# Kernel tuning notes

Measured on AMD Instinct MI355X. Metric: run time of the kernel, lower is better.

The kernel has to match this reference:

```python
import jax, jax.numpy as jnp
import numpy as np

H = 16  # num_attention_heads


def setup_inputs() -> dict:
    key = jax.random.key(0)
    ks = jax.random.split(key, 4)
    B, S, D = 2, 2048, 1024
    hidden_states = jax.random.normal(ks[0], (B, S, D), dtype=jnp.float32)
    attention_mask = jnp.zeros((B, 1, 1, S), dtype=jnp.float32)
    scale = 1.0 / np.sqrt(D)
    Wq = jax.random.normal(ks[1], (D, D), dtype=jnp.float32) * scale
    Wk = jax.random.normal(ks[2], (D, D), dtype=jnp.float32) * scale
    Wv = jax.random.normal(ks[3], (D, D), dtype=jnp.float32) * scale
    bq = jnp.zeros((D,), dtype=jnp.float32)
    bk = jnp.zeros((D,), dtype=jnp.float32)
    bv = jnp.zeros((D,), dtype=jnp.float32)
    return {"hidden_states": hidden_states, "attention_mask": attention_mask,
            "Wq": Wq, "bq": bq, "Wk": Wk, "bk": bk, "Wv": Wv, "bv": bv}


def reference(hidden_states, attention_mask, Wq, bq, Wk, bk, Wv, bv):
    B, S, D = hidden_states.shape
    Dh = D // H

    def proj(W, b):
        # torch Linear: x @ W.T + b ; reshape to [B, H, S, Dh]
        y = jnp.einsum('bsd,ed->bse', hidden_states, W) + b
        return y.reshape(B, S, H, Dh).transpose(0, 2, 1, 3)

    q = proj(Wq, bq)
    k = proj(Wk, bk)
    v = proj(Wv, bv)

    scores = jnp.einsum('bhqd,bhkd->bhqk', q, k) / jnp.sqrt(jnp.float32(Dh))
    scores = scores + attention_mask  # additive mask broadcast [B,1,1,S]
    probs = jax.nn.softmax(scores, axis=-1)  # [B,H,Sq,Sk]
    out_attention_scores = probs.sum(axis=-2).sum(axis=-2)  # [B, Sk]
    # dropout prob = 0 (eval) -> identity
    context = jnp.einsum('bhqk,bhkd->bhqd', probs, v)
    context = context.transpose(0, 2, 1, 3).reshape(B, S, D)
    return context, out_attention_scores
```

## Files before the change

### kernel.cpp

```cpp
#include <hip/hip_runtime.h>
#include <hip/hip_bf16.h>
#include <stdint.h>

typedef unsigned short u16;
typedef __attribute__((ext_vector_type(8))) unsigned short u16x8;
typedef __attribute__((ext_vector_type(4))) unsigned short u16x4;
typedef __attribute__((ext_vector_type(8))) __bf16 bf16x8;
typedef __attribute__((ext_vector_type(4))) float f32x4;
typedef __attribute__((ext_vector_type(16))) float f32x16;

#define LOG2E 1.44269504088896340736f

#if defined(__has_builtin)
#if __has_builtin(__builtin_amdgcn_exp2f)
#define EXP2(x) __builtin_amdgcn_exp2f(x)
#endif
#endif
#ifndef EXP2
#define EXP2(x) exp2f(x)
#endif

__device__ __forceinline__ f32x4 mfma16(u16x8 a, u16x8 b, f32x4 c) {
  return __builtin_amdgcn_mfma_f32_16x16x32_bf16(
      __builtin_bit_cast(bf16x8, a), __builtin_bit_cast(bf16x8, b), c, 0, 0, 0);
}

__device__ __forceinline__ f32x16 mfma32(u16x8 a, u16x8 b, f32x16 c) {
  return __builtin_amdgcn_mfma_f32_32x32x16_bf16(
      __builtin_bit_cast(bf16x8, a), __builtin_bit_cast(bf16x8, b), c, 0, 0, 0);
}

__device__ __forceinline__ u16 f2bf(float f) {
  unsigned u = __builtin_bit_cast(unsigned, f);
  return (u16)((u + 0x7fffu + ((u >> 16) & 1u)) >> 16);
}

__device__ __forceinline__ unsigned cvtpk(float a, float b) {
  unsigned r;
  asm volatile("v_cvt_pk_bf16_f32 %0, %1, %2" : "=v"(r) : "v"(a), "v"(b));
  return r;
}

__device__ __forceinline__ void pswap(unsigned& a, unsigned& b) {
  asm volatile("v_permlane32_swap_b32 %0, %1" : "+v"(a), "+v"(b));
}

__device__ __forceinline__ void gload_lds16(const void* g, void* l) {
  __builtin_amdgcn_global_load_lds(
      (__attribute__((address_space(1))) void*)const_cast<void*>(g),
      (__attribute__((address_space(3))) void*)l, 16, 0, 0);
}

template<int N> __device__ __forceinline__ void vmwait() {
  __builtin_amdgcn_sched_barrier(0);
  asm volatile("s_waitcnt vmcnt(%0)" :: "n"(N) : "memory");
  __builtin_amdgcn_sched_barrier(0);
}

#define SWZ(row, colbyte) ((((row) * 128) + (colbyte)) ^ (((row) & 7) << 4))

__global__ void cast_all(const float* __restrict__ X,
                         const float* __restrict__ s0, const float* __restrict__ s1,
                         const float* __restrict__ s2, const float* __restrict__ mask,
                         u16* __restrict__ Xb, u16* __restrict__ Wcat,
                         float* __restrict__ maskL, float* __restrict__ out_cs) {
  const int bid = blockIdx.x;
  if (bid >= 7168) {
    const int i = (bid - 7168) * 256 + threadIdx.x;
    f32x4 m = ((const f32x4*)mask)[i];
    m[0] *= LOG2E; m[1] *= LOG2E; m[2] *= LOG2E; m[3] *= LOG2E;
    ((f32x4*)maskL)[i] = m;
    f32x4 z = {0.f, 0.f, 0.f, 0.f};
    ((f32x4*)out_cs)[i] = z;
    return;
  }
  const float* src;
  u16* dst;
  int i;
  if (bid < 4096) {
    src = X; dst = Xb;
    i = bid * 256 + threadIdx.x;
  } else {
    const int wb = bid - 4096;
    const int seg = wb >> 10;
    src = (seg == 0) ? s0 : ((seg == 1) ? s1 : s2);
    dst = Wcat + (size_t)seg * 1048576;
    i = (wb & 1023) * 256 + threadIdx.x;
  }
  f32x4 v = ((const f32x4*)src)[i];
  u16x4 o;
  o[0] = f2bf(v[0]); o[1] = f2bf(v[1]); o[2] = f2bf(v[2]); o[3] = f2bf(v[3]);
  ((u16x4*)dst)[i] = o;
}

__global__ __launch_bounds__(256) void gemm_qkv(
    const u16* __restrict__ A, const u16* __restrict__ Bm,
    const float* __restrict__ bq, const float* __restrict__ bk, const float* __restrict__ bv,
    u16* __restrict__ Qb, u16* __restrict__ Kb, u16* __restrict__ VTb) {
  __shared__ __align__(16) u16 Asm[3][4096];
  __shared__ __align__(16) u16 Bsm[3][4096];
  const int tid = threadIdx.x;
  const int wave = tid >> 6, lane = tid & 63;
  const int lq = lane & 15, lg = lane >> 4;
  const int wr = wave >> 1, wc = wave & 1;
  const int lin = blockIdx.y * 24 + blockIdx.x;
  const int wg = (lin & 7) * 96 + (lin >> 3);
  const int m0 = (wg / 24) * 128, n0 = (wg % 24) * 128;

  f32x4 zero = {0.f, 0.f, 0.f, 0.f};
  f32x4 acc[4][4];
#pragma unroll
  for (int mi = 0; mi < 4; ++mi)
#pragma unroll
    for (int ni = 0; ni < 4; ++ni) acc[mi][ni] = zero;

  int rA0, k16A0, rA1, k16A1;
  {
    const int cc0 = wave * 128 + lane;
    const int ln0 = cc0 >> 3, sp0 = (cc0 & 7) ^ (ln0 & 7);
    rA0 = ln0 * 2 + (sp0 >> 2); k16A0 = sp0 & 3;
    const int cc1 = cc0 + 64;
    const int ln1 = cc1 >> 3, sp1 = (cc1 & 7) ^ (ln1 & 7);
    rA1 = ln1 * 2 + (sp1 >> 2); k16A1 = sp1 & 3;
  }

  auto stage = [&](int kt, int buf) {
    const int kk = kt * 32;
    gload_lds16(A + (size_t)(m0 + rA0) * 1024 + kk + k16A0 * 8,
                (char*)&Asm[buf][0] + (wave * 2 + 0) * 1024);
    gload_lds16(A + (size_t)(m0 + rA1) * 1024 + kk + k16A1 * 8,
                (char*)&Asm[buf][0] + (wave * 2 + 1) * 1024);
    gload_lds16(Bm + (size_t)(n0 + rA0) * 1024 + kk + k16A0 * 8,
                (char*)&Bsm[buf][0] + (wave * 2 + 0) * 1024);
    gload_lds16(Bm + (size_t)(n0 + rA1) * 1024 + kk + k16A1 * 8,
                (char*)&Bsm[buf][0] + (wave * 2 + 1) * 1024);
  };

  stage(0, 0);
  stage(1, 1);
  for (int kt = 0; kt < 32; ++kt) {
    if (kt < 31) vmwait<4>(); else vmwait<0>();
    __builtin_amdgcn_s_barrier();
    if (kt + 2 < 32) stage(kt + 2, (kt + 2) % 3);
    const int cur = kt % 3;

    __builtin_amdgcn_s_setprio(1);
    u16x8 af[4], bfr[4];
#pragma unroll
    for (int mi = 0; mi < 4; ++mi) {
      const int rA = wr * 64 + mi * 16 + lq;
      const int lnA = rA >> 1;
      const int spA = ((rA & 1) << 2) | lg;
      af[mi] = *(const u16x8*)((const char*)&Asm[cur][0] +
                               lnA * 128 + ((spA ^ (lnA & 7)) << 4));
    }
#pragma unroll
    for (int ni = 0; ni < 4; ++ni) {
      const int rB = wc * 64 + ni * 16 + lq;
      const int lnB = rB >> 1;
      const int spB = ((rB & 1) << 2) | lg;
      bfr[ni] = *(const u16x8*)((const char*)&Bsm[cur][0] +
                                lnB * 128 + ((spB ^ (lnB & 7)) << 4));
    }
#pragma unroll
    for (int mi = 0; mi < 4; ++mi)
#pragma unroll
      for (int ni = 0; ni < 4; ++ni)
        acc[mi][ni] = mfma16(af[mi], bfr[ni], acc[mi][ni]);
    __builtin_amdgcn_s_setprio(0);
  }

  const int which = n0 >> 10;
  const float* bias = (which == 0) ? bq : ((which == 1) ? bk : bv);
  const float scl = (which == 0) ? (0.125f * LOG2E) : 1.0f;
#pragma unroll
  for (int mi = 0; mi < 4; ++mi) {
    const int m = m0 + wr * 64 + mi * 16 + lg * 4;
    const int bb = m >> 11;
    const int s = m & 2047;
#pragma unroll
    for (int ni = 0; ni < 4; ++ni) {
      const int n = n0 + wc * 64 + ni * 16 + lq;
      const int d = n & 1023;
      const int h = d >> 6, dh = d & 63;
      const float bi = bias[d];
#pragma unroll
      for (int r = 0; r < 4; ++r) {
        float v = (acc[mi][ni][r] + bi) * scl;
        if (which == 2)
          VTb[(((size_t)bb * 16 + h) * 64 + dh) * 2048 + (size_t)(s + r)] = f2bf(v);
        else {
          u16* dst = (which == 0) ? Qb : Kb;
          dst[(((size_t)bb * 16 + h) * 2048 + (size_t)(s + r)) * 64 + dh] = f2bf(v);
        }
      }
    }
  }
}

__global__ __launch_bounds__(512) void attn_pair(
    const u16* __restrict__ Qb, const u16* __restrict__ Kb, const u16* __restrict__ VTb,
    const float* __restrict__ maskL, float* __restrict__ out_ctx, float* __restrict__ winv) {
  __shared__ __align__(16) char smem[57344];

  const int tid = threadIdx.x;
  const int w = tid >> 6, lane = tid & 63;
  const int l31 = lane & 31, h = lane >> 5;
  const int hf = w >> 2, p = w & 3;
  const int bid = (blockIdx.x & 7) * 64 + (blockIdx.x >> 3);
  const int qt = bid & 15, bh = bid >> 4;
  const int b = bh >> 4, hh = bh & 15;
  const int qw = qt * 128 + p * 32;

  float* maskLds = (float*)(smem + 49152);
  {
    const f32x4 m = ((const f32x4*)(maskL + b * 2048))[tid];
    *(f32x4*)(maskLds + tid * 4) = m;
  }

  const u16* qp = Qb + ((size_t)bh * 2048 + qw + l31) * 64 + h * 8;
  u16x8 qa[4];
#pragma unroll
  for (int dq = 0; dq < 4; ++dq) qa[dq] = *(const u16x8*)(qp + dq * 16);

  const char* KbaseG = (const char*)(Kb + (size_t)bh * 2048 * 64);
  const char* VTbaseG = (const char*)(VTb + (size_t)bh * 64 * 2048);

  const int t8 = tid & 255;
  const int srowK = t8 >> 3;
  const int scolK = ((t8 & 7) * 16) ^ ((srowK & 7) << 4);
  const int lineV = t8 >> 3;
  const int spV = (t8 & 7) ^ (lineV & 7);
  const int dhV = lineV * 2 + (spV >> 2);
  const int kbV = (spV & 3) * 16;

  auto stage = [&](int kt, int buf) {
    char* kd = smem + hf * 12288 + buf * 4096 + (w & 3) * 1024;
    gload_lds16(KbaseG + (size_t)(kt * 32 + srowK) * 128 + scolK, kd);
    char* vd = smem + 24576 + hf * 12288 + buf * 4096 + (w & 3) * 1024;
    gload_lds16(VTbaseG + (size_t)dhV * 4096 + (size_t)kt * 64 + kbV, vd);
  };

  f32x16 accpv[2];
#pragma unroll
  for (int db = 0; db < 2; ++db)
#pragma unroll
    for (int r = 0; r < 16; ++r) accpv[db][r] = 0.f;
  float l_l = 0.f;

  __syncthreads();
  const int kt0 = hf * 32;
  stage(kt0, 0);
  stage(kt0 + 1, 1);
  for (int j = 0; j < 32; ++j) {
    const int kt = kt0 + j;
    if (j < 31) vmwait<2>(); else vmwait<0>();
    __builtin_amdgcn_s_barrier();
    const char* Kt = smem + hf * 12288 + (j % 3) * 4096;
    const char* Vt = smem + 24576 + hf * 12288 + (j % 3) * 4096;

    __builtin_amdgcn_s_setprio(1);
    f32x16 s;
    {
      const float* mrow = maskLds + kt * 32 + h * 4;
#pragma unroll
      for (int g = 0; g < 4; ++g) {
        const f32x4 mv = *(const f32x4*)(mrow + g * 8);
        s[g * 4 + 0] = mv[0]; s[g * 4 + 1] = mv[1];
        s[g * 4 + 2] = mv[2]; s[g * 4 + 3] = mv[3];
      }
    }
#pragma unroll
    for (int dq = 0; dq < 4; ++dq) {
      const u16x8 ka = *(const u16x8*)(Kt + SWZ(l31, dq * 32 + h * 16));
      s = mfma32(ka, qa[dq], s);
    }
    float pv[16];
#pragma unroll
    for (int r = 0; r < 16; ++r) pv[r] = EXP2(s[r]);
    l_l += ((pv[0] + pv[1]) + (pv[2] + pv[3])) + ((pv[4] + pv[5]) + (pv[6] + pv[7])) +
           ((pv[8] + pv[9]) + (pv[10] + pv[11])) + ((pv[12] + pv[13]) + (pv[14] + pv[15]));
    unsigned a01 = cvtpk(pv[0], pv[1]), a23 = cvtpk(pv[2], pv[3]);
    unsigned a45 = cvtpk(pv[4], pv[5]), a67 = cvtpk(pv[6], pv[7]);
    unsigned b01 = cvtpk(pv[8], pv[9]), b23 = cvtpk(pv[10], pv[11]);
    unsigned b45 = cvtpk(pv[12], pv[13]), b67 = cvtpk(pv[14], pv[15]);
    pswap(a01, a45); pswap(a23, a67);
    pswap(b01, b45); pswap(b23, b67);
    uint4 f1 = {a01, a23, a45, a67};
    uint4 f2 = {b01, b23, b45, b67};
    u16x8 pf[2] = {__builtin_bit_cast(u16x8, f1), __builtin_bit_cast(u16x8, f2)};
#pragma unroll
    for (int ks2 = 0; ks2 < 2; ++ks2) {
#pragma unroll
      for (int db = 0; db < 2; ++db) {
        const int rowV = db * 32 + l31;
        const int lnV = rowV >> 1;
        const int sV = ((rowV & 1) << 2) | (ks2 << 1) | h;
        const u16x8 vt = *(const u16x8*)(Vt + lnV * 128 + ((sV ^ (lnV & 7)) << 4));
        accpv[db] = mfma32(pf[ks2], vt, accpv[db]);
      }
    }
    __builtin_amdgcn_s_setprio(0);
    __builtin_amdgcn_sched_barrier(0);
    if (j + 2 < 32) stage(kt0 + j + 2, (j + 2) % 3);
  }

  l_l += __shfl_xor(l_l, 32);

  __syncthreads();
  float* pairctx = (float*)smem;
  float* pairl = (float*)(smem + 32768);
  if (hf == 1) {
#pragma unroll
    for (int db = 0; db < 2; ++db)
#pragma unroll
      for (int r = 0; r < 16; ++r) {
        const int q = (r & 3) + (r >> 2) * 8 + h * 4;
        pairctx[p * 2048 + q * 64 + db * 32 + l31] = accpv[db][r];
      }
    if (h == 0) pairl[p * 32 + l31] = l_l;
  }
  __syncthreads();
  if (hf == 0) {
    const float lt = l_l + pairl[p * 32 + l31];
    const float il = 1.0f / lt;
    if (h == 0) winv[bh * 2048 + qw + l31] = il;
#pragma unroll
    for (int r = 0; r < 16; ++r) {
      const int q = (r & 3) + (r >> 2) * 8 + h * 4;
      const float ilr = __shfl(il, q);
      const size_t row = (size_t)(b * 2048 + qw + q) * 1024 + hh * 64;
      out_ctx[row + l31] = (accpv[0][r] + pairctx[p * 2048 + q * 64 + l31]) * ilr;
      out_ctx[row + 32 + l31] = (accpv[1][r] + pairctx[p * 2048 + q * 64 + 32 + l31]) * ilr;
    }
  }
}

__global__ __launch_bounds__(256) void colsum_kernel(
    const u16* __restrict__ Qb, const u16* __restrict__ Kb,
    const float* __restrict__ maskL, const float* __restrict__ winv,
    float* __restrict__ out_cs) {
  __shared__ __align__(16) u16 Ql[3][4096];
  __shared__ float winvLds[512];

  const int tid = threadIdx.x;
  const int w = tid >> 6, lane = tid & 63;
  const int lq = lane & 15, lg = lane >> 4;
  const int bid = (blockIdx.x & 7) * 128 + (blockIdx.x >> 3);
  const int ktile = bid & 7, qq = (bid >> 3) & 3, bh = bid >> 5;
  const int b = bh >> 4;
  const int kbase = ktile * 256 + w * 64;
  const int q0t = qq * 8;

  if (tid < 128) {
    const f32x4 v = ((const f32x4*)(winv + (size_t)bh * 2048 + q0t * 64))[tid];
    *(f32x4*)(winvLds + tid * 4) = v;
  }

  const u16* kp = Kb + ((size_t)bh * 2048 + kbase + lq) * 64 + lg * 8;
  u16x8 kf[4][2];
  f32x4 zg[4];
#pragma unroll
  for (int g = 0; g < 4; ++g) {
    kf[g][0] = *(const u16x8*)(kp + (size_t)g * 16 * 64);
    kf[g][1] = *(const u16x8*)(kp + (size_t)g * 16 * 64 + 32);
    const float m = maskL[b * 2048 + kbase + g * 16 + lq];
    zg[g][0] = m; zg[g][1] = m; zg[g][2] = m; zg[g][3] = m;
  }
  const char* Qbase = (const char*)(Qb + (size_t)bh * 2048 * 64);

  const int r0 = tid >> 3;
  const int scol = ((tid & 7) * 16) ^ ((r0 & 7) << 4);
  auto stageQ = [&](int qt, int buf) {
    const char* src = Qbase + (size_t)(qt * 64) * 128;
    char* d = (char*)&Ql[buf][0] + w * 1024;
    gload_lds16(src + (size_t)r0 * 128 + scol, d);
    gload_lds16(src + (size_t)(r0 + 32) * 128 + scol, d + 4096);
  };

  float c0 = 0.f, c1 = 0.f, c2 = 0.f, c3 = 0.f;
  __syncthreads();
  stageQ(q0t, 0);
  stageQ(q0t + 1, 1);
  for (int j = 0; j < 8; ++j) {
    if (j < 7) vmwait<2>(); else vmwait<0>();
    __builtin_amdgcn_s_barrier();
    const char* Qt = (const char*)&Ql[j % 3][0];
    __builtin_amdgcn_s_setprio(1);
#pragma unroll
    for (int chunk = 0; chunk < 4; ++chunk) {
      const u16x8 qf0 = *(const u16x8*)(Qt + SWZ(chunk * 16 + lq, lg * 16));
      const u16x8 qf1 = *(const u16x8*)(Qt + SWZ(chunk * 16 + lq, 64 + lg * 16));
      const f32x4 wv = *(const f32x4*)(winvLds + j * 64 + chunk * 16 + lg * 4);
      f32x4 s0 = mfma16(qf0, kf[0][0], zg[0]); s0 = mfma16(qf1, kf[0][1], s0);
      f32x4 s1 = mfma16(qf0, kf[1][0], zg[1]); s1 = mfma16(qf1, kf[1][1], s1);
      f32x4 s2 = mfma16(qf0, kf[2][0], zg[2]); s2 = mfma16(qf1, kf[2][1], s2);
      f32x4 s3 = mfma16(qf0, kf[3][0], zg[3]); s3 = mfma16(qf1, kf[3][1], s3);
#pragma unroll
      for (int r = 0; r < 4; ++r) {
        c0 = fmaf(EXP2(s0[r]), wv[r], c0);
        c1 = fmaf(EXP2(s1[r]), wv[r], c1);
        c2 = fmaf(EXP2(s2[r]), wv[r], c2);
        c3 = fmaf(EXP2(s3[r]), wv[r], c3);
      }
    }
    __builtin_amdgcn_s_setprio(0);
    __builtin_amdgcn_sched_barrier(0);
    if (j + 2 < 8) stageQ(q0t + j + 2, (j + 2) % 3);
  }
  c0 += __shfl_xor(c0, 16); c0 += __shfl_xor(c0, 32);
  c1 += __shfl_xor(c1, 16); c1 += __shfl_xor(c1, 32);
  c2 += __shfl_xor(c2, 16); c2 += __shfl_xor(c2, 32);
  c3 += __shfl_xor(c3, 16); c3 += __shfl_xor(c3, 32);
  if (lg == 0) {
    atomicAdd(&out_cs[b * 2048 + kbase + lq], c0);
    atomicAdd(&out_cs[b * 2048 + kbase + 16 + lq], c1);
    atomicAdd(&out_cs[b * 2048 + kbase + 32 + lq], c2);
    atomicAdd(&out_cs[b * 2048 + kbase + 48 + lq], c3);
  }
}

extern "C" void kernel_launch(void* const* d_in, const int* in_sizes, int n_in,
                              void* d_out, int out_size, void* d_ws, size_t ws_size,
                              hipStream_t stream) {
  (void)in_sizes; (void)n_in; (void)out_size; (void)ws_size;
  const float* X    = (const float*)d_in[0];
  const float* mask = (const float*)d_in[1];
  const float* Wq   = (const float*)d_in[2];
  const float* bq   = (const float*)d_in[3];
  const float* Wk   = (const float*)d_in[4];
  const float* bk   = (const float*)d_in[5];
  const float* Wv   = (const float*)d_in[6];
  const float* bv   = (const float*)d_in[7];
  float* out = (float*)d_out;

  char* ws = (char*)d_ws;
  u16* Xb   = (u16*)(ws);
  u16* Wcat = (u16*)(ws + 8388608);
  u16* Qb   = (u16*)(ws + 14680064);
  u16* Kb   = (u16*)(ws + 23068672);
  u16* VTb  = (u16*)(ws + 31457280);
  float* winv  = (float*)(ws + 39845888);
  float* maskL = (float*)(ws + 40108032);

  cast_all<<<7172, 256, 0, stream>>>(X, Wq, Wk, Wv, mask, Xb, Wcat,
                                     maskL, out + 4194304);

  gemm_qkv<<<dim3(24, 32), 256, 0, stream>>>(Xb, Wcat, bq, bk, bv, Qb, Kb, VTb);

  attn_pair<<<512, 512, 0, stream>>>(Qb, Kb, VTb, maskL, out, winv);
  colsum_kernel<<<1024, 256, 0, stream>>>(Qb, Kb, maskL, winv, out + 4194304);
}
```

Before: 127.5 us.

## Compute softmax row sums via MFMA and retile colsum kernel for more K reuse

The attention kernel now gets the softmax denominator from two extra MFMAs that multiply the bf16 probabilities by a ones matrix, replacing a chain of VALU adds and a cross-lane shuffle. The row sums now come from the bf16-rounded probabilities, matching the values used in the PV product. The colsum kernel now has each wave hold 128 keys in registers and loop over half as many Q tiles, which halves Q reloads per key. It also factors the mask out as a per-key exp2 multiplier instead of seeding the MFMA accumulator with it. The cost is higher register pressure and fewer blocks per key range.

```diff
diff --git a/kernel.cpp b/kernel.cpp
--- a/kernel.cpp
+++ b/kernel.cpp
@@ -241,12 +241,17 @@
     gload_lds16(VTbaseG + (size_t)dhV * 4096 + (size_t)kt * 64 + kbV, vd);
   };
 
-  f32x16 accpv[2];
+  f32x16 accpv[2], lacc;
 #pragma unroll
   for (int db = 0; db < 2; ++db)
 #pragma unroll
     for (int r = 0; r < 16; ++r) accpv[db][r] = 0.f;
-  float l_l = 0.f;
+#pragma unroll
+  for (int r = 0; r < 16; ++r) lacc[r] = 0.f;
+
+  const unsigned o2 = 0x3F803F80u;
+  uint4 ov = {o2, o2, o2, o2};
+  const u16x8 onesf = __builtin_bit_cast(u16x8, ov);
 
   __syncthreads();
   const int kt0 = hf * 32;
@@ -278,8 +283,6 @@
     float pv[16];
 #pragma unroll
     for (int r = 0; r < 16; ++r) pv[r] = EXP2(s[r]);
-    l_l += ((pv[0] + pv[1]) + (pv[2] + pv[3])) + ((pv[4] + pv[5]) + (pv[6] + pv[7])) +
-           ((pv[8] + pv[9]) + (pv[10] + pv[11])) + ((pv[12] + pv[13]) + (pv[14] + pv[15]));
     unsigned a01 = cvtpk(pv[0], pv[1]), a23 = cvtpk(pv[2], pv[3]);
     unsigned a45 = cvtpk(pv[4], pv[5]), a67 = cvtpk(pv[6], pv[7]);
     unsigned b01 = cvtpk(pv[8], pv[9]), b23 = cvtpk(pv[10], pv[11]);
@@ -289,6 +292,8 @@
     uint4 f1 = {a01, a23, a45, a67};
     uint4 f2 = {b01, b23, b45, b67};
     u16x8 pf[2] = {__builtin_bit_cast(u16x8, f1), __builtin_bit_cast(u16x8, f2)};
+    lacc = mfma32(pf[0], onesf, lacc);
+    lacc = mfma32(pf[1], onesf, lacc);
 #pragma unroll
     for (int ks2 = 0; ks2 < 2; ++ks2) {
 #pragma unroll
@@ -305,8 +310,6 @@
     if (j + 2 < 32) stage(kt0 + j + 2, (j + 2) % 3);
   }
 
-  l_l += __shfl_xor(l_l, 32);
-
   __syncthreads();
   float* pairctx = (float*)smem;
   float* pairl = (float*)(smem + 32768);
@@ -318,20 +321,36 @@
         const int q = (r & 3) + (r >> 2) * 8 + h * 4;
         pairctx[p * 2048 + q * 64 + db * 32 + l31] = accpv[db][r];
       }
-    if (h == 0) pairl[p * 32 + l31] = l_l;
+    if (l31 == 0) {
+#pragma unroll
+      for (int r = 0; r < 16; ++r) {
+        const int q = (r & 3) + (r >> 2) * 8 + h * 4;
+        pairl[p * 32 + q] = lacc[r];
+      }
+    }
   }
   __syncthreads();
   if (hf == 0) {
-    const float lt = l_l + pairl[p * 32 + l31];
-    const float il = 1.0f / lt;
-    if (h == 0) winv[bh * 2048 + qw + l31] = il;
+    f32x4 plv[4];
+#pragma unroll
+    for (int g = 0; g < 4; ++g)
+      plv[g] = *(const f32x4*)&pairl[p * 32 + g * 8 + h * 4];
+    float il[16];
+#pragma unroll
+    for (int r = 0; r < 16; ++r) il[r] = 1.0f / (lacc[r] + plv[r >> 2][r & 3]);
+    if (l31 == 0) {
+#pragma unroll
+      for (int r = 0; r < 16; ++r) {
+        const int q = (r & 3) + (r >> 2) * 8 + h * 4;
+        winv[bh * 2048 + qw + q] = il[r];
+      }
+    }
 #pragma unroll
     for (int r = 0; r < 16; ++r) {
       const int q = (r & 3) + (r >> 2) * 8 + h * 4;
-      const float ilr = __shfl(il, q);
       const size_t row = (size_t)(b * 2048 + qw + q) * 1024 + hh * 64;
-      out_ctx[row + l31] = (accpv[0][r] + pairctx[p * 2048 + q * 64 + l31]) * ilr;
-      out_ctx[row + 32 + l31] = (accpv[1][r] + pairctx[p * 2048 + q * 64 + 32 + l31]) * ilr;
+      out_ctx[row + l31] = (accpv[0][r] + pairctx[p * 2048 + q * 64 + l31]) * il[r];
+      out_ctx[row + 32 + l31] = (accpv[1][r] + pairctx[p * 2048 + q * 64 + 32 + l31]) * il[r];
     }
   }
 }
@@ -341,31 +360,30 @@
     const float* __restrict__ maskL, const float* __restrict__ winv,
     float* __restrict__ out_cs) {
   __shared__ __align__(16) u16 Ql[3][4096];
-  __shared__ float winvLds[512];
+  __shared__ float winvLds[256];
 
   const int tid = threadIdx.x;
   const int w = tid >> 6, lane = tid & 63;
   const int lq = lane & 15, lg = lane >> 4;
   const int bid = (blockIdx.x & 7) * 128 + (blockIdx.x >> 3);
-  const int ktile = bid & 7, qq = (bid >> 3) & 3, bh = bid >> 5;
+  const int ktile = bid & 3, qq = (bid >> 2) & 7, bh = bid >> 5;
   const int b = bh >> 4;
-  const int kbase = ktile * 256 + w * 64;
-  const int q0t = qq * 8;
-
-  if (tid < 128) {
+  const int kbase = ktile * 512 + w * 128;
+  const int q0t = qq * 4;
+
+  if (tid < 64) {
     const f32x4 v = ((const f32x4*)(winv + (size_t)bh * 2048 + q0t * 64))[tid];
     *(f32x4*)(winvLds + tid * 4) = v;
   }
 
   const u16* kp = Kb + ((size_t)bh * 2048 + kbase + lq) * 64 + lg * 8;
-  u16x8 kf[4][2];
-  f32x4 zg[4];
-#pragma unroll
-  for (int g = 0; g < 4; ++g) {
+  u16x8 kf[8][2];
+  float wm[8];
+#pragma unroll
+  for (int g = 0; g < 8; ++g) {
     kf[g][0] = *(const u16x8*)(kp + (size_t)g * 16 * 64);
     kf[g][1] = *(const u16x8*)(kp + (size_t)g * 16 * 64 + 32);
-    const float m = maskL[b * 2048 + kbase + g * 16 + lq];
-    zg[g][0] = m; zg[g][1] = m; zg[g][2] = m; zg[g][3] = m;
+    wm[g] = EXP2(maskL[b * 2048 + kbase + g * 16 + lq]);
   }
   const char* Qbase = (const char*)(Qb + (size_t)bh * 2048 * 64);
 
@@ -378,12 +396,16 @@
     gload_lds16(src + (size_t)(r0 + 32) * 128 + scol, d + 4096);
   };
 
-  float c0 = 0.f, c1 = 0.f, c2 = 0.f, c3 = 0.f;
+  float c[8];
+#pragma unroll
+  for (int g = 0; g < 8; ++g) c[g] = 0.f;
+  const f32x4 zf = {0.f, 0.f, 0.f, 0.f};
+
   __syncthreads();
   stageQ(q0t, 0);
   stageQ(q0t + 1, 1);
-  for (int j = 0; j < 8; ++j) {
-    if (j < 7) vmwait<2>(); else vmwait<0>();
+  for (int j = 0; j < 4; ++j) {
+    if (j < 3) vmwait<2>(); else vmwait<0>();
     __builtin_amdgcn_s_barrier();
     const char* Qt = (const char*)&Ql[j % 3][0];
     __builtin_amdgcn_s_setprio(1);
@@ -392,31 +414,28 @@
       const u16x8 qf0 = *(const u16x8*)(Qt + SWZ(chunk * 16 + lq, lg * 16));
       const u16x8 qf1 = *(const u16x8*)(Qt + SWZ(chunk * 16 + lq, 64 + lg * 16));
       const f32x4 wv = *(const f32x4*)(winvLds + j * 64 + chunk * 16 + lg * 4);
-      f32x4 s0 = mfma16(qf0, kf[0][0], zg[0]); s0 = mfma16(qf1, kf[0][1], s0);
-      f32x4 s1 = mfma16(qf0, kf[1][0], zg[1]); s1 = mfma16(qf1, kf[1][1], s1);
-      f32x4 s2 = mfma16(qf0, kf[2][0], zg[2]); s2 = mfma16(qf1, kf[2][1], s2);
-      f32x4 s3 = mfma16(qf0, kf[3][0], zg[3]); s3 = mfma16(qf1, kf[3][1], s3);
-#pragma unroll
-      for (int r = 0; r < 4; ++r) {
-        c0 = fmaf(EXP2(s0[r]), wv[r], c0);
-        c1 = fmaf(EXP2(s1[r]), wv[r], c1);
-        c2 = fmaf(EXP2(s2[r]), wv[r], c2);
-        c3 = fmaf(EXP2(s3[r]), wv[r], c3);
+#pragma unroll
+      for (int g = 0; g < 8; ++g) {
+        f32x4 sg = mfma16(qf0, kf[g][0], zf);
+        sg = mfma16(qf1, kf[g][1], sg);
+#pragma unroll
+        for (int r = 0; r < 4; ++r) c[g] = fmaf(EXP2(sg[r]), wv[r], c[g]);
       }
     }
     __builtin_amdgcn_s_setprio(0);
     __builtin_amdgcn_sched_barrier(0);
-    if (j + 2 < 8) stageQ(q0t + j + 2, (j + 2) % 3);
-  }
-  c0 += __shfl_xor(c0, 16); c0 += __shfl_xor(c0, 32);
-  c1 += __shfl_xor(c1, 16); c1 += __shfl_xor(c1, 32);
-  c2 += __shfl_xor(c2, 16); c2 += __shfl_xor(c2, 32);
-  c3 += __shfl_xor(c3, 16); c3 += __shfl_xor(c3, 32);
+    if (j + 2 < 4) stageQ(q0t + j + 2, (j + 2) % 3);
+  }
+#pragma unroll
+  for (int g = 0; g < 8; ++g) {
+    c[g] *= wm[g];
+    c[g] += __shfl_xor(c[g], 16);
+    c[g] += __shfl_xor(c[g], 32);
+  }
   if (lg == 0) {
-    atomicAdd(&out_cs[b * 2048 + kbase + lq], c0);
-    atomicAdd(&out_cs[b * 2048 + kbase + 16 + lq], c1);
-    atomicAdd(&out_cs[b * 2048 + kbase + 32 + lq], c2);
-    atomicAdd(&out_cs[b * 2048 + kbase + 48 + lq], c3);
+#pragma unroll
+    for (int g = 0; g < 8; ++g)
+      atomicAdd(&out_cs[b * 2048 + kbase + g * 16 + lq], c[g]);
   }
 }
 
```

New measurement: 129.3 us. About the same (+1.4%).

## Deepen attention K/V prefetch to four stages and compute row sums via MFMA

Applied to the files above, without the earlier changes.

The attention kernel's K/V LDS ring grows from three to four buffers. The next tile's loads are now issued right after the barrier instead of after the compute, so three tiles are in flight. The softmax row-sum moves from scalar VALU adds plus a cross-lane shuffle to two extra MFMAs against an all-ones bf16 operand; the final normalisation then reads per-row sums straight from the accumulator layout. The colsum kernel likewise issues its Q prefetch before the compute. The cost is more LDS per block, which could hurt occupancy, and two extra matrix ops per iteration in exchange for fewer vector ALU instructions.

```diff
diff --git a/kernel.cpp b/kernel.cpp
--- a/kernel.cpp
+++ b/kernel.cpp
@@ -201,7 +201,7 @@
 __global__ __launch_bounds__(512) void attn_pair(
     const u16* __restrict__ Qb, const u16* __restrict__ Kb, const u16* __restrict__ VTb,
     const float* __restrict__ maskL, float* __restrict__ out_ctx, float* __restrict__ winv) {
-  __shared__ __align__(16) char smem[57344];
+  __shared__ __align__(16) char smem[73728];
 
   const int tid = threadIdx.x;
   const int w = tid >> 6, lane = tid & 63;
@@ -212,7 +212,7 @@
   const int b = bh >> 4, hh = bh & 15;
   const int qw = qt * 128 + p * 32;
 
-  float* maskLds = (float*)(smem + 49152);
+  float* maskLds = (float*)(smem + 65536);
   {
     const f32x4 m = ((const f32x4*)(maskL + b * 2048))[tid];
     *(f32x4*)(maskLds + tid * 4) = m;
@@ -235,29 +235,36 @@
   const int kbV = (spV & 3) * 16;
 
   auto stage = [&](int kt, int buf) {
-    char* kd = smem + hf * 12288 + buf * 4096 + (w & 3) * 1024;
+    char* kd = smem + hf * 16384 + buf * 4096 + (w & 3) * 1024;
     gload_lds16(KbaseG + (size_t)(kt * 32 + srowK) * 128 + scolK, kd);
-    char* vd = smem + 24576 + hf * 12288 + buf * 4096 + (w & 3) * 1024;
+    char* vd = smem + 32768 + hf * 16384 + buf * 4096 + (w & 3) * 1024;
     gload_lds16(VTbaseG + (size_t)dhV * 4096 + (size_t)kt * 64 + kbV, vd);
   };
 
-  f32x16 accpv[2];
+  f32x16 accpv[2], lacc;
 #pragma unroll
   for (int db = 0; db < 2; ++db)
 #pragma unroll
     for (int r = 0; r < 16; ++r) accpv[db][r] = 0.f;
-  float l_l = 0.f;
+#pragma unroll
+  for (int r = 0; r < 16; ++r) lacc[r] = 0.f;
+
+  const unsigned o2 = 0x3F803F80u;
+  uint4 ov = {o2, o2, o2, o2};
+  const u16x8 onesf = __builtin_bit_cast(u16x8, ov);
 
   __syncthreads();
   const int kt0 = hf * 32;
   stage(kt0, 0);
   stage(kt0 + 1, 1);
+  stage(kt0 + 2, 2);
   for (int j = 0; j < 32; ++j) {
     const int kt = kt0 + j;
-    if (j < 31) vmwait<2>(); else vmwait<0>();
+    if (j < 30) vmwait<4>(); else if (j == 30) vmwait<2>(); else vmwait<0>();
     __builtin_amdgcn_s_barrier();
-    const char* Kt = smem + hf * 12288 + (j % 3) * 4096;
-    const char* Vt = smem + 24576 + hf * 12288 + (j % 3) * 4096;
+    if (j + 3 < 32) stage(kt0 + j + 3, (j + 3) & 3);
+    const char* Kt = smem + hf * 16384 + (j & 3) * 4096;
+    const char* Vt = smem + 32768 + hf * 16384 + (j & 3) * 4096;
 
     __builtin_amdgcn_s_setprio(1);
     f32x16 s;
@@ -278,8 +285,6 @@
     float pv[16];
 #pragma unroll
     for (int r = 0; r < 16; ++r) pv[r] = EXP2(s[r]);
-    l_l += ((pv[0] + pv[1]) + (pv[2] + pv[3])) + ((pv[4] + pv[5]) + (pv[6] + pv[7])) +
-           ((pv[8] + pv[9]) + (pv[10] + pv[11])) + ((pv[12] + pv[13]) + (pv[14] + pv[15]));
     unsigned a01 = cvtpk(pv[0], pv[1]), a23 = cvtpk(pv[2], pv[3]);
     unsigned a45 = cvtpk(pv[4], pv[5]), a67 = cvtpk(pv[6], pv[7]);
     unsigned b01 = cvtpk(pv[8], pv[9]), b23 = cvtpk(pv[10], pv[11]);
@@ -289,6 +294,8 @@
     uint4 f1 = {a01, a23, a45, a67};
     uint4 f2 = {b01, b23, b45, b67};
     u16x8 pf[2] = {__builtin_bit_cast(u16x8, f1), __builtin_bit_cast(u16x8, f2)};
+    lacc = mfma32(pf[0], onesf, lacc);
+    lacc = mfma32(pf[1], onesf, lacc);
 #pragma unroll
     for (int ks2 = 0; ks2 < 2; ++ks2) {
 #pragma unroll
@@ -302,10 +309,7 @@
     }
     __builtin_amdgcn_s_setprio(0);
     __builtin_amdgcn_sched_barrier(0);
-    if (j + 2 < 32) stage(kt0 + j + 2, (j + 2) % 3);
-  }
-
-  l_l += __shfl_xor(l_l, 32);
+  }
 
   __syncthreads();
   float* pairctx = (float*)smem;
@@ -318,20 +322,36 @@
         const int q = (r & 3) + (r >> 2) * 8 + h * 4;
         pairctx[p * 2048 + q * 64 + db * 32 + l31] = accpv[db][r];
       }
-    if (h == 0) pairl[p * 32 + l31] = l_l;
+    if (l31 == 0) {
+#pragma unroll
+      for (int r = 0; r < 16; ++r) {
+        const int q = (r & 3) + (r >> 2) * 8 + h * 4;
+        pairl[p * 32 + q] = lacc[r];
+      }
+    }
   }
   __syncthreads();
   if (hf == 0) {
-    const float lt = l_l + pairl[p * 32 + l31];
-    const float il = 1.0f / lt;
-    if (h == 0) winv[bh * 2048 + qw + l31] = il;
+    f32x4 plv[4];
+#pragma unroll
+    for (int g = 0; g < 4; ++g)
+      plv[g] = *(const f32x4*)&pairl[p * 32 + g * 8 + h * 4];
+    float il[16];
+#pragma unroll
+    for (int r = 0; r < 16; ++r) il[r] = 1.0f / (lacc[r] + plv[r >> 2][r & 3]);
+    if (l31 == 0) {
+#pragma unroll
+      for (int r = 0; r < 16; ++r) {
+        const int q = (r & 3) + (r >> 2) * 8 + h * 4;
+        winv[bh * 2048 + qw + q] = il[r];
+      }
+    }
 #pragma unroll
     for (int r = 0; r < 16; ++r) {
       const int q = (r & 3) + (r >> 2) * 8 + h * 4;
-      const float ilr = __shfl(il, q);
       const size_t row = (size_t)(b * 2048 + qw + q) * 1024 + hh * 64;
-      out_ctx[row + l31] = (accpv[0][r] + pairctx[p * 2048 + q * 64 + l31]) * ilr;
-      out_ctx[row + 32 + l31] = (accpv[1][r] + pairctx[p * 2048 + q * 64 + 32 + l31]) * ilr;
+      out_ctx[row + l31] = (accpv[0][r] + pairctx[p * 2048 + q * 64 + l31]) * il[r];
+      out_ctx[row + 32 + l31] = (accpv[1][r] + pairctx[p * 2048 + q * 64 + 32 + l31]) * il[r];
     }
   }
 }
@@ -385,6 +405,7 @@
   for (int j = 0; j < 8; ++j) {
     if (j < 7) vmwait<2>(); else vmwait<0>();
     __builtin_amdgcn_s_barrier();
+    if (j + 2 < 8) stageQ(q0t + j + 2, (j + 2) % 3);
     const char* Qt = (const char*)&Ql[j % 3][0];
     __builtin_amdgcn_s_setprio(1);
 #pragma unroll
@@ -406,7 +427,6 @@
     }
     __builtin_amdgcn_s_setprio(0);
     __builtin_amdgcn_sched_barrier(0);
-    if (j + 2 < 8) stageQ(q0t + j + 2, (j + 2) % 3);
   }
   c0 += __shfl_xor(c0, 16); c0 += __shfl_xor(c0, 32);
   c1 += __shfl_xor(c1, 16); c1 += __shfl_xor(c1, 32);
```

New measurement: 130.0 us. Within noise of the previous version (+1.9%).
